# Performance work log

Measured on AMD Instinct MI355X. Metric: run time of the kernel, lower is better.

The kernel has to match this reference:

```python
import jax, jax.numpy as jnp
import numpy as np

D_STATE = 8
D_CONV = 4
DT_RANK = 8
THRESHOLD = 0.5
KPOOL = 3
PAD = (KPOOL - 1) // 2
EPS = 1e-5


def _rmsnorm(x, w):
    return x * jax.lax.rsqrt(jnp.mean(x * x, axis=-1, keepdims=True) + EPS) * w


def _dw_causal_conv(x, w, b):
    # x: (L, T, C), w: (C, 1, K) depthwise causal conv along T
    xt = jnp.transpose(x, (0, 2, 1))  # (L, C, T)
    y = jax.lax.conv_general_dilated(
        xt, w, window_strides=(1,), padding=[(D_CONV - 1, 0)],
        dimension_numbers=('NCH', 'OIH', 'NCH'), feature_group_count=xt.shape[1])
    return jnp.transpose(y, (0, 2, 1)) + b


def _selective_scan(x, delta, A, B, Cm, D):
    # x, delta: (L,T,d); A: (d,n); B, Cm: (L,T,n); D: (d,)
    dA = jnp.exp(delta[..., None] * A)                        # (L,T,d,n)
    dBx = (delta * x)[..., None] * B[:, :, None, :]           # (L,T,d,n)
    def combine(a, b):
        a1, b1 = a
        a2, b2 = b
        return (a2 * a1, a2 * b1 + b2)
    _, h = jax.lax.associative_scan(combine, (dA, dBx), axis=1)
    y = jnp.einsum('ltdn,ltn->ltd', h, Cm)
    return y + x * D


def _mamba_block(x, in_proj, conv_w, conv_b, x_proj_w, dt_proj_w, dt_proj_b,
                 A_log_f, A_log_b, D_f, D_b, out_proj_w, rms_w):
    # single-depth bidirectional (bimamba-v2 style) block, expand=1, residual + RMSNorm
    res = x
    xn = _rmsnorm(x, rms_w)
    xz = xn @ in_proj                       # (L,T,2C)
    xi, z = jnp.split(xz, 2, axis=-1)
    xi = jax.nn.silu(_dw_causal_conv(xi, conv_w, conv_b))
    dbl = xi @ x_proj_w                     # (L,T,dt_rank+2*d_state)
    dt = dbl[..., :DT_RANK]
    Bm = dbl[..., DT_RANK:DT_RANK + D_STATE]
    Cm = dbl[..., DT_RANK + D_STATE:]
    delta = jax.nn.softplus(dt @ dt_proj_w + dt_proj_b)
    A_f = -jnp.exp(A_log_f)
    A_b = -jnp.exp(A_log_b)
    flip = lambda a: a[:, ::-1]
    y_f = _selective_scan(xi, delta, A_f, Bm, Cm, D_f)
    y_b = flip(_selective_scan(flip(xi), flip(delta), A_b, flip(Bm), flip(Cm), D_b))
    y = 0.5 * (y_f + y_b) * jax.nn.silu(z)  # if_devide_out -> average two directions
    return res + y @ out_proj_w


def reference(feats, in_proj, conv_w, conv_b, x_proj_w, dt_proj_w, dt_proj_b,
              A_log_f, A_log_b, D_f, D_b, out_proj_w, rms_w, mlp_w, mlp_b,
              record_len):
    N, C, H, W = feats.shape
    T = H * W
    rec = np.asarray(record_len)  # static ragged group sizes
    ends = np.cumsum(rec)
    starts = ends - rec
    masks = []
    for s0, L in zip(starts.tolist(), rec.tolist()):
        g = feats[s0:s0 + L]                       # (L,C,H,W)
        if L > 1:
            x = g.reshape(L, C, T).transpose(0, 2, 1)  # l c h w -> l (h w) c
            feat = _mamba_block(x, in_proj, conv_w, conv_b, x_proj_w, dt_proj_w,
                                dt_proj_b, A_log_f, A_log_b, D_f, D_b,
                                out_proj_w, rms_w)
            score = jax.nn.sigmoid(feat @ mlp_w + mlp_b)   # (L,T,1)
            ego = jnp.ones((1, T, 1), feats.dtype)
            bs = jnp.concatenate([ego, score[1:]], axis=0)
        else:
            bs = jnp.ones((1, T, 1), feats.dtype)
        bs = bs.transpose(0, 2, 1).reshape(L, 1, H, W)     # l (h w) c -> l c h w
        masks.append(jnp.where(bs > THRESHOLD, 1.0, 0.0).astype(feats.dtype))
    mask = jnp.concatenate(masks, axis=0)                  # (N,1,H,W)
    pooled = jax.lax.reduce_window(
        mask, -jnp.inf, jax.lax.max,
        window_dimensions=(1, 1, KPOOL, KPOOL), window_strides=(1, 1, 1, 1),
        padding=[(0, 0), (0, 0), (PAD, PAD), (PAD, PAD)])
    return pooled


def setup_inputs():
    key = jax.random.key(0)
    ks = jax.random.split(key, 8)
    C, H, W = 128, 96, 96
    record_len = np.array([2, 3, 1, 2, 4], dtype=np.int64)
    N = int(record_len.sum())
    s = 0.05
    A_log = jnp.log(jnp.broadcast_to(
        jnp.arange(1, D_STATE + 1, dtype=jnp.float32), (C, D_STATE)))
    return {
        'feats': jax.random.normal(ks[0], (N, C, H, W), jnp.float32),
        'in_proj': jax.random.normal(ks[1], (C, 2 * C), jnp.float32) * s,
        'conv_w': jax.random.normal(ks[2], (C, 1, D_CONV), jnp.float32) * s,
        'conv_b': jnp.zeros((C,), jnp.float32),
        'x_proj_w': jax.random.normal(ks[3], (C, DT_RANK + 2 * D_STATE), jnp.float32) * s,
        'dt_proj_w': jax.random.normal(ks[4], (DT_RANK, C), jnp.float32) * s,
        'dt_proj_b': jnp.full((C,), 0.1, jnp.float32),
        'A_log_f': A_log,
        'A_log_b': A_log,
        'D_f': jnp.ones((C,), jnp.float32),
        'D_b': jnp.ones((C,), jnp.float32),
        'out_proj_w': jax.random.normal(ks[5], (C, C), jnp.float32) * s,
        'rms_w': jnp.ones((C,), jnp.float32),
        'mlp_w': jax.random.normal(ks[6], (C, 1), jnp.float32) * s,
        'mlp_b': jnp.zeros((1,), jnp.float32),
        'record_len': jnp.asarray(record_len),
    }
```

## Files before the change

kernel.cpp:

```cpp
#include <hip/hip_runtime.h>
#include <cstdint>
#include <cstddef>

#define C_CH 128
#define T_TOK 9216
#define H_IMG 96
#define W_IMG 96
#define NSTATE 8

#define CHUNK 64
#define RHALO 32
#define REGION (CHUNK + 2 * RHALO)

__device__ __forceinline__ float siluf_dev(float x) {
  return x / (1.0f + expf(-x));
}

__device__ __forceinline__ float fast_silu(float x) {
  return __fdividef(x, 1.0f + __expf(-x));
}

__global__ __launch_bounds__(128) void k0_setup(
    const int* __restrict__ rec, int n_groups, int N,
    const float* __restrict__ out_proj_w, const float* __restrict__ mlp_w,
    float* __restrict__ vvec, int* __restrict__ slot)
{
  const int tid = threadIdx.x;
  if (tid == 0) {
    int f = 0, sl = 0;
    for (int g = 0; g < n_groups; ++g) {
      const int L = rec[g];
      slot[f] = -1;
      for (int i = 1; i < L; ++i) slot[f + i] = sl++;
      f += L;
    }
  }
  if (tid < C_CH) {
    float acc = 0.0f;
    for (int j = 0; j < C_CH; ++j) acc += out_proj_w[tid * C_CH + j] * mlp_w[j];
    vvec[tid] = acc;
  }
}

__global__ __launch_bounds__(256) void k1_gemm(
    const float* __restrict__ feats, const float* __restrict__ in_proj,
    const float* __restrict__ rms_w, const float* __restrict__ mlp_w,
    const float* __restrict__ mlp_b, const float* __restrict__ vvec,
    const int* __restrict__ slot,
    float* __restrict__ xipre, float* __restrict__ wbuf,
    float* __restrict__ logit)
{
  __shared__ float Asm[C_CH * 64];
  __shared__ float Bsm[C_CH * 64];
  __shared__ float redA[256], redB[256], irS[64];
  const int f = blockIdx.y;
  const int s = slot[f];
  if (s < 0) return;
  const int m0 = blockIdx.x * 64;
  const int tid = threadIdx.x;

  {
    const int c0 = tid >> 4;
    const int tq = (tid & 15) * 4;
    const float* src = feats + (size_t)f * C_CH * T_TOK + m0 + tq;
    #pragma unroll
    for (int i = 0; i < 8; ++i) {
      const int c = c0 + i * 16;
      const float4 x4 = *(const float4*)(src + (size_t)c * T_TOK);
      *(float4*)&Asm[c * 64 + tq] = x4;
    }
  }
  __syncthreads();
  {
    const int t = tid & 63;
    const int q = tid >> 6;
    float ssum = 0.0f, rm = 0.0f;
    for (int cc = q * 32; cc < q * 32 + 32; ++cc) {
      const float val = Asm[cc * 64 + t];
      ssum += val * val;
      rm += val * mlp_w[cc];
    }
    redA[tid] = ssum; redB[tid] = rm;
  }
  __syncthreads();
  if (tid < 64) {
    const int t = tid;
    const float ssum = redA[t] + redA[t + 64] + redA[t + 128] + redA[t + 192];
    const float rm   = redB[t] + redB[t + 64] + redB[t + 128] + redB[t + 192];
    const float ir = 1.0f / sqrtf(ssum * (1.0f / C_CH) + 1e-5f);
    logit[(size_t)s * T_TOK + m0 + t] = rm + mlp_b[0];
    irS[t] = ir;
  }
  __syncthreads();
  {
    const int t = tid & 63;
    const int q = tid >> 6;
    const float ir = irS[t];
    for (int cc = q * 32; cc < q * 32 + 32; ++cc) Asm[cc * 64 + t] *= ir;
  }

  const int ti = tid >> 4;
  const int tc = tid & 15;
  for (int chunk = 0; chunk < 4; ++chunk) {
    const int n0 = chunk * 64;
    __syncthreads();
    #pragma unroll
    for (int i = 0; i < 8; ++i) {
      const int idx = tid + 256 * i;
      const int k = idx >> 4;
      const int q = (idx & 15) * 4;
      float4 b4 = *(const float4*)(in_proj + (size_t)k * 256 + n0 + q);
      const float rw = rms_w[k];
      b4.x *= rw; b4.y *= rw; b4.z *= rw; b4.w *= rw;
      *(float4*)&Bsm[k * 64 + q] = b4;
    }
    __syncthreads();
    float acc[4][4];
    #pragma unroll
    for (int i = 0; i < 4; ++i)
      #pragma unroll
      for (int j = 0; j < 4; ++j) acc[i][j] = 0.0f;
    #pragma unroll 8
    for (int k = 0; k < C_CH; ++k) {
      const float4 a4 = *(const float4*)&Asm[k * 64 + ti * 4];
      const float4 b4 = *(const float4*)&Bsm[k * 64 + tc * 4];
      acc[0][0] += a4.x * b4.x; acc[0][1] += a4.x * b4.y; acc[0][2] += a4.x * b4.z; acc[0][3] += a4.x * b4.w;
      acc[1][0] += a4.y * b4.x; acc[1][1] += a4.y * b4.y; acc[1][2] += a4.y * b4.z; acc[1][3] += a4.y * b4.w;
      acc[2][0] += a4.z * b4.x; acc[2][1] += a4.z * b4.y; acc[2][2] += a4.z * b4.z; acc[2][3] += a4.z * b4.w;
      acc[3][0] += a4.w * b4.x; acc[3][1] += a4.w * b4.y; acc[3][2] += a4.w * b4.z; acc[3][3] += a4.w * b4.w;
    }
    if (chunk < 2) {
      const int cb = n0 + tc * 4;
      #pragma unroll
      for (int i = 0; i < 4; ++i) {
        const int t = m0 + ti * 4 + i;
        float4 o; o.x = acc[i][0]; o.y = acc[i][1]; o.z = acc[i][2]; o.w = acc[i][3];
        *(float4*)&xipre[((size_t)s * T_TOK + t) * C_CH + cb] = o;
      }
    } else {
      const int zc = (chunk - 2) * 64 + tc * 4;
      const float4 v4 = *(const float4*)&vvec[zc];
      #pragma unroll
      for (int i = 0; i < 4; ++i) {
        const int t = m0 + ti * 4 + i;
        float4 o;
        o.x = 0.5f * siluf_dev(acc[i][0]) * v4.x;
        o.y = 0.5f * siluf_dev(acc[i][1]) * v4.y;
        o.z = 0.5f * siluf_dev(acc[i][2]) * v4.z;
        o.w = 0.5f * siluf_dev(acc[i][3]) * v4.w;
        *(float4*)&wbuf[((size_t)s * T_TOK + t) * C_CH + zc] = o;
      }
    }
  }
}

__global__ __launch_bounds__(256, 4) void k2_convproj(
    const float* __restrict__ xipre,
    const float* __restrict__ conv_w, const float* __restrict__ conv_b,
    const float* __restrict__ x_proj_w, const int* __restrict__ slot,
    float* __restrict__ dbl_g)
{
  __shared__ float xibuf[64 * 129];
  const int f = blockIdx.y;
  const int s = slot[f];
  if (s < 0) return;
  const int m0 = blockIdx.x * 64;
  const int tid = threadIdx.x;
  const int c = tid & 127;
  const int half = tid >> 7;
  const size_t rowbase = (size_t)s * T_TOK;
  const float4 cw = *(const float4*)(conv_w + c * 4);
  const float cb = conv_b[c];

  auto ldx = [&](int t) -> float {
    return (t >= 0) ? xipre[(rowbase + t) * C_CH + c] : 0.0f;
  };

  {
    const int t0 = m0 + half * 32;
    float xm1 = ldx(t0 - 1), xm2 = ldx(t0 - 2), xm3 = ldx(t0 - 3);
    #pragma unroll
    for (int i = 0; i < 32; ++i) {
      const float cur = ldx(t0 + i);
      const float sum = cw.x * xm3 + cw.y * xm2 + cw.z * xm1 + cw.w * cur + cb;
      xibuf[(half * 32 + i) * 129 + c] = fast_silu(sum);
      xm3 = xm2; xm2 = xm1; xm1 = cur;
    }
  }
  __syncthreads();
  {
    const int q6 = __builtin_amdgcn_readfirstlane(tid >> 6) * 6;
    const int tok = tid & 63;
    float acc[6] = {0, 0, 0, 0, 0, 0};
    for (int cc = 0; cc < C_CH; ++cc) {
      const float xv = xibuf[tok * 129 + cc];
      #pragma unroll
      for (int jj = 0; jj < 6; ++jj)
        acc[jj] += xv * x_proj_w[cc * 24 + q6 + jj];
    }
    #pragma unroll
    for (int jj = 0; jj < 6; ++jj)
      dbl_g[(rowbase + m0 + tok) * 24 + q6 + jj] = acc[jj];
  }
}

__global__ __launch_bounds__(256, 4) void k3_scan(
    const float* __restrict__ xipre, const float* __restrict__ wbuf,
    const float* __restrict__ dbl_g,
    const float* __restrict__ conv_w, const float* __restrict__ conv_b,
    const float* __restrict__ dt_proj_w, const float* __restrict__ dt_proj_b,
    const float* __restrict__ A_log_f, const float* __restrict__ A_log_b,
    const float* __restrict__ D_f, const float* __restrict__ D_b,
    const int* __restrict__ slot, float* __restrict__ logit)
{
  __shared__ float dbl[REGION * 24];
  const int f = blockIdx.y;
  const int s = slot[f];
  if (s < 0) return;
  const int c0 = blockIdx.x * CHUNK;
  const int r0 = c0 - RHALO;
  const int tid = threadIdx.x;
  const int c = tid & 127;
  const int half = tid >> 7;
  const size_t rowbase = (size_t)s * T_TOK;
  const float4 cw = *(const float4*)(conv_w + c * 4);
  const float cb = conv_b[c];

  auto ldx = [&](int t) -> float {
    return (t >= 0 && t < T_TOK) ? xipre[(rowbase + t) * C_CH + c] : 0.0f;
  };

  {
    const long grow = ((long)rowbase + r0) * 24;
    const int lo  = (r0 < 0) ? (-r0) * 6 : 0;
    const int hi  = (r0 + REGION > T_TOK) ? (T_TOK - r0) * 6 : REGION * 6;
    #pragma unroll
    for (int i = 0; i < 3; ++i) {
      const int idx = tid + i * 256;
      if (idx >= lo && idx < hi)
        *(float4*)&dbl[idx * 4] = *(const float4*)&dbl_g[grow + (long)idx * 4];
    }
  }
  __syncthreads();

  float dw[8], Ac[8];
  const float* Alog = half ? A_log_b : A_log_f;
  #pragma unroll
  for (int r = 0; r < 8; ++r) dw[r] = dt_proj_w[r * C_CH + c];
  #pragma unroll
  for (int n = 0; n < NSTATE; ++n) Ac[n] = -expf(Alog[c * NSTATE + n]);
  const float bias = dt_proj_b[c];
  const float Dd = half ? D_b[c] : D_f[c];
  float h[8] = {0, 0, 0, 0, 0, 0, 0, 0};

  const float a0 = Ac[0];
  int okl = 1;
  #pragma unroll
  for (int n = 1; n < NSTATE; ++n)
    okl &= (fabsf(Ac[n] - (float)(n + 1) * a0) <= 1e-4f * fabsf(Ac[n])) ? 1 : 0;
  const bool fastA = (__all(okl) != 0);

  auto decay8 = [&](float dlt, float* dA) {
    if (fastA) {
      const float e1 = __expf(dlt * a0);
      const float e2 = e1 * e1, e3 = e2 * e1, e4 = e2 * e2;
      dA[0] = e1; dA[1] = e2; dA[2] = e3; dA[3] = e4;
      dA[4] = e4 * e1; dA[5] = e4 * e2; dA[6] = e4 * e3; dA[7] = e4 * e4;
    } else {
      #pragma unroll
      for (int n = 0; n < NSTATE; ++n) dA[n] = __expf(dlt * Ac[n]);
    }
  };

  if (half == 0) {
    const int tb = (r0 < 0) ? 0 : r0;
    const int steps = c0 + CHUNK - tb;
    const int outg0 = (c0 - tb) >> 3;
    const int ng = steps >> 3;
    float xm1 = ldx(tb - 1), xm2 = ldx(tb - 2), xm3 = ldx(tb - 3);
    for (int g = 0; g < ng; ++g) {
      const int t0 = tb + g * 8;
      const bool out = (g >= outg0);
      float pg[8], wg[8];
      #pragma unroll
      for (int j = 0; j < 8; ++j) {
        const size_t gi = (rowbase + t0 + j) * C_CH + c;
        pg[j] = xipre[gi];
        wg[j] = out ? wbuf[gi] : 0.0f;
      }
      #pragma unroll
      for (int j = 0; j < 8; ++j) {
        const int t = t0 + j;
        const int p = t - r0;
        const float cur = pg[j];
        const float sum = cw.x * xm3 + cw.y * xm2 + cw.z * xm1 + cw.w * cur + cb;
        const float xiv = fast_silu(sum);
        xm3 = xm2; xm2 = xm1; xm1 = cur;
        const float4 d0 = *(const float4*)&dbl[p * 24];
        const float4 d1 = *(const float4*)&dbl[p * 24 + 4];
        float pre = bias;
        pre += d0.x * dw[0] + d0.y * dw[1] + d0.z * dw[2] + d0.w * dw[3];
        pre += d1.x * dw[4] + d1.y * dw[5] + d1.z * dw[6] + d1.w * dw[7];
        const float dlt = fmaxf(pre, 0.0f) + __logf(1.0f + __expf(-fabsf(pre)));
        const float u = dlt * xiv;
        const float4 b0 = *(const float4*)&dbl[p * 24 + 8];
        const float4 b1 = *(const float4*)&dbl[p * 24 + 12];
        float dA[8];
        decay8(dlt, dA);
        h[0] = dA[0] * h[0] + u * b0.x;
        h[1] = dA[1] * h[1] + u * b0.y;
        h[2] = dA[2] * h[2] + u * b0.z;
        h[3] = dA[3] * h[3] + u * b0.w;
        h[4] = dA[4] * h[4] + u * b1.x;
        h[5] = dA[5] * h[5] + u * b1.y;
        h[6] = dA[6] * h[6] + u * b1.z;
        h[7] = dA[7] * h[7] + u * b1.w;
        if (out) {
          const float4 cc0 = *(const float4*)&dbl[p * 24 + 16];
          const float4 cc1 = *(const float4*)&dbl[p * 24 + 20];
          float y = xiv * Dd;
          y += h[0] * cc0.x + h[1] * cc0.y + h[2] * cc0.z + h[3] * cc0.w;
          y += h[4] * cc1.x + h[5] * cc1.y + h[6] * cc1.z + h[7] * cc1.w;
          float contrib = y * wg[j];
          contrib += __shfl_xor(contrib, 1);
          contrib += __shfl_xor(contrib, 2);
          contrib += __shfl_xor(contrib, 4);
          contrib += __shfl_xor(contrib, 8);
          contrib += __shfl_xor(contrib, 16);
          contrib += __shfl_xor(contrib, 32);
          if ((tid & 63) == 0) atomicAdd(&logit[rowbase + t], contrib);
        }
      }
    }
  } else {
    const int te2e = r0 + REGION;
    const int te2 = (te2e > T_TOK) ? T_TOK : te2e;
    const int steps = te2 - c0;
    const int outg0 = (te2 - (c0 + CHUNK)) >> 3;
    const int ng = steps >> 3;
    float w0 = ldx(te2 - 1), w1 = ldx(te2 - 2), w2 = ldx(te2 - 3), w3 = ldx(te2 - 4);
    for (int g = 0; g < ng; ++g) {
      const int t0 = te2 - 1 - g * 8;
      const bool out = (g >= outg0);
      float nv[8], wg[8];
      #pragma unroll
      for (int j = 0; j < 8; ++j) {
        nv[j] = ldx(t0 - 4 - j);
        wg[j] = out ? wbuf[(rowbase + t0 - j) * C_CH + c] : 0.0f;
      }
      #pragma unroll
      for (int j = 0; j < 8; ++j) {
        const int t = t0 - j;
        const int p = t - r0;
        const float sum = cw.x * w3 + cw.y * w2 + cw.z * w1 + cw.w * w0 + cb;
        const float xiv = fast_silu(sum);
        w0 = w1; w1 = w2; w2 = w3; w3 = nv[j];
        const float4 d0 = *(const float4*)&dbl[p * 24];
        const float4 d1 = *(const float4*)&dbl[p * 24 + 4];
        float pre = bias;
        pre += d0.x * dw[0] + d0.y * dw[1] + d0.z * dw[2] + d0.w * dw[3];
        pre += d1.x * dw[4] + d1.y * dw[5] + d1.z * dw[6] + d1.w * dw[7];
        const float dlt = fmaxf(pre, 0.0f) + __logf(1.0f + __expf(-fabsf(pre)));
        const float u = dlt * xiv;
        const float4 b0 = *(const float4*)&dbl[p * 24 + 8];
        const float4 b1 = *(const float4*)&dbl[p * 24 + 12];
        float dA[8];
        decay8(dlt, dA);
        h[0] = dA[0] * h[0] + u * b0.x;
        h[1] = dA[1] * h[1] + u * b0.y;
        h[2] = dA[2] * h[2] + u * b0.z;
        h[3] = dA[3] * h[3] + u * b0.w;
        h[4] = dA[4] * h[4] + u * b1.x;
        h[5] = dA[5] * h[5] + u * b1.y;
        h[6] = dA[6] * h[6] + u * b1.z;
        h[7] = dA[7] * h[7] + u * b1.w;
        if (out) {
          const float4 cc0 = *(const float4*)&dbl[p * 24 + 16];
          const float4 cc1 = *(const float4*)&dbl[p * 24 + 20];
          float y = xiv * Dd;
          y += h[0] * cc0.x + h[1] * cc0.y + h[2] * cc0.z + h[3] * cc0.w;
          y += h[4] * cc1.x + h[5] * cc1.y + h[6] * cc1.z + h[7] * cc1.w;
          float contrib = y * wg[j];
          contrib += __shfl_xor(contrib, 1);
          contrib += __shfl_xor(contrib, 2);
          contrib += __shfl_xor(contrib, 4);
          contrib += __shfl_xor(contrib, 8);
          contrib += __shfl_xor(contrib, 16);
          contrib += __shfl_xor(contrib, 32);
          if ((tid & 63) == 0) atomicAdd(&logit[rowbase + t], contrib);
        }
      }
    }
  }
}

__global__ __launch_bounds__(128) void k4_pool(
    const float* __restrict__ logit, const int* __restrict__ slot,
    float* __restrict__ out)
{
  const int w = threadIdx.x;
  if (w >= W_IMG) return;
  const int hh = blockIdx.x;
  const int f = blockIdx.y;
  const int s = slot[f];
  float m = 0.0f;
  if (s < 0) {
    m = 1.0f;
  } else {
    for (int dh = -1; dh <= 1; ++dh) {
      const int h2 = hh + dh;
      if (h2 < 0 || h2 >= H_IMG) continue;
      for (int dw = -1; dw <= 1; ++dw) {
        const int w2 = w + dw;
        if (w2 < 0 || w2 >= W_IMG) continue;
        if (logit[(size_t)s * T_TOK + h2 * W_IMG + w2] > 0.0f) m = 1.0f;
      }
    }
  }
  out[(size_t)f * T_TOK + hh * W_IMG + w] = m;
}

extern "C" void kernel_launch(void* const* d_in, const int* in_sizes, int n_in,
                              void* d_out, int out_size, void* d_ws, size_t ws_size,
                              hipStream_t stream) {
  const float* feats      = (const float*)d_in[0];
  const float* in_proj    = (const float*)d_in[1];
  const float* conv_w     = (const float*)d_in[2];
  const float* conv_b     = (const float*)d_in[3];
  const float* x_proj_w   = (const float*)d_in[4];
  const float* dt_proj_w  = (const float*)d_in[5];
  const float* dt_proj_b  = (const float*)d_in[6];
  const float* A_log_f    = (const float*)d_in[7];
  const float* A_log_b    = (const float*)d_in[8];
  const float* D_f        = (const float*)d_in[9];
  const float* D_b        = (const float*)d_in[10];
  const float* out_proj_w = (const float*)d_in[11];
  const float* rms_w      = (const float*)d_in[12];
  const float* mlp_w      = (const float*)d_in[13];
  const float* mlp_b      = (const float*)d_in[14];
  const int*   rec        = (const int*)d_in[15];

  const int N = in_sizes[0] / (C_CH * T_TOK);
  const int n_groups = in_sizes[15];
  int S = N - n_groups;
  if (S < 1) S = 1;

  char* p = (char*)d_ws;
  float* vvec  = (float*)p; p += 1024;
  int*   slot  = (int*)p;   p += ((N * 4 + 255) / 256) * 256;
  float* logit = (float*)p; p += (size_t)S * T_TOK * 4;
  float* xipre = (float*)p; p += (size_t)S * T_TOK * C_CH * 4;
  float* wA    = (float*)p; p += (size_t)S * T_TOK * C_CH * 4;
  float* dblg  = (float*)p; p += (size_t)S * T_TOK * 24 * 4;
  (void)ws_size; (void)n_in; (void)out_size;

  k0_setup<<<1, 128, 0, stream>>>(rec, n_groups, N, out_proj_w, mlp_w, vvec, slot);
  k1_gemm<<<dim3(T_TOK / 64, N), 256, 0, stream>>>(
      feats, in_proj, rms_w, mlp_w, mlp_b, vvec, slot, xipre, wA, logit);
  k2_convproj<<<dim3(T_TOK / 64, N), 256, 0, stream>>>(
      xipre, conv_w, conv_b, x_proj_w, slot, dblg);
  k3_scan<<<dim3(T_TOK / CHUNK, N), 256, 0, stream>>>(
      xipre, wA, dblg, conv_w, conv_b, dt_proj_w, dt_proj_b,
      A_log_f, A_log_b, D_f, D_b, slot, logit);
  k4_pool<<<dim3(H_IMG, N), 128, 0, stream>>>(logit, slot, (float*)d_out);
}
```

Baseline: 323.3 us.

## Split scan directions across blocks, double-buffer scan loads, drop GEMM B staging

The scan kernel now runs forward and backward directions as separate 128-thread blocks along a grid z dimension instead of two halves of one 256-thread block. Its per-group global loads are double-buffered so the next 8-token group is fetched while the current one is processed. The input-projection GEMM stops staging in_proj in shared memory; it folds rms_w into the A tile and reads B directly from global/L2, freeing shared memory for higher occupancy. The risks are higher register pressure from the doubled load buffers and more global traffic per FMA in the GEMM.

```diff
diff --git a/kernel.cpp b/kernel.cpp
--- a/kernel.cpp
+++ b/kernel.cpp
@@ -42,7 +42,7 @@
   }
 }
 
-__global__ __launch_bounds__(256) void k1_gemm(
+__global__ __launch_bounds__(256, 4) void k1_gemm(
     const float* __restrict__ feats, const float* __restrict__ in_proj,
     const float* __restrict__ rms_w, const float* __restrict__ mlp_w,
     const float* __restrict__ mlp_b, const float* __restrict__ vvec,
@@ -51,7 +51,6 @@
     float* __restrict__ logit)
 {
   __shared__ float Asm[C_CH * 64];
-  __shared__ float Bsm[C_CH * 64];
   __shared__ float redA[256], redB[256], irS[64];
   const int f = blockIdx.y;
   const int s = slot[f];
@@ -96,25 +95,16 @@
     const int t = tid & 63;
     const int q = tid >> 6;
     const float ir = irS[t];
-    for (int cc = q * 32; cc < q * 32 + 32; ++cc) Asm[cc * 64 + t] *= ir;
-  }
+    for (int cc = q * 32; cc < q * 32 + 32; ++cc)
+      Asm[cc * 64 + t] = (Asm[cc * 64 + t] * ir) * rms_w[cc];
+  }
+  __syncthreads();
 
   const int ti = tid >> 4;
   const int tc = tid & 15;
   for (int chunk = 0; chunk < 4; ++chunk) {
     const int n0 = chunk * 64;
-    __syncthreads();
-    #pragma unroll
-    for (int i = 0; i < 8; ++i) {
-      const int idx = tid + 256 * i;
-      const int k = idx >> 4;
-      const int q = (idx & 15) * 4;
-      float4 b4 = *(const float4*)(in_proj + (size_t)k * 256 + n0 + q);
-      const float rw = rms_w[k];
-      b4.x *= rw; b4.y *= rw; b4.z *= rw; b4.w *= rw;
-      *(float4*)&Bsm[k * 64 + q] = b4;
-    }
-    __syncthreads();
+    const float* bp = in_proj + n0 + tc * 4;
     float acc[4][4];
     #pragma unroll
     for (int i = 0; i < 4; ++i)
@@ -123,7 +113,7 @@
     #pragma unroll 8
     for (int k = 0; k < C_CH; ++k) {
       const float4 a4 = *(const float4*)&Asm[k * 64 + ti * 4];
-      const float4 b4 = *(const float4*)&Bsm[k * 64 + tc * 4];
+      const float4 b4 = *(const float4*)(bp + (size_t)k * 256);
       acc[0][0] += a4.x * b4.x; acc[0][1] += a4.x * b4.y; acc[0][2] += a4.x * b4.z; acc[0][3] += a4.x * b4.w;
       acc[1][0] += a4.y * b4.x; acc[1][1] += a4.y * b4.y; acc[1][2] += a4.y * b4.z; acc[1][3] += a4.y * b4.w;
       acc[2][0] += a4.z * b4.x; acc[2][1] += a4.z * b4.y; acc[2][2] += a4.z * b4.z; acc[2][3] += a4.z * b4.w;
@@ -204,7 +194,7 @@
   }
 }
 
-__global__ __launch_bounds__(256, 4) void k3_scan(
+__global__ __launch_bounds__(128, 4) void k3_scan(
     const float* __restrict__ xipre, const float* __restrict__ wbuf,
     const float* __restrict__ dbl_g,
     const float* __restrict__ conv_w, const float* __restrict__ conv_b,
@@ -220,8 +210,8 @@
   const int c0 = blockIdx.x * CHUNK;
   const int r0 = c0 - RHALO;
   const int tid = threadIdx.x;
-  const int c = tid & 127;
-  const int half = tid >> 7;
+  const int c = tid;
+  const int half = blockIdx.z;
   const size_t rowbase = (size_t)s * T_TOK;
   const float4 cw = *(const float4*)(conv_w + c * 4);
   const float cb = conv_b[c];
@@ -235,8 +225,8 @@
     const int lo  = (r0 < 0) ? (-r0) * 6 : 0;
     const int hi  = (r0 + REGION > T_TOK) ? (T_TOK - r0) * 6 : REGION * 6;
     #pragma unroll
-    for (int i = 0; i < 3; ++i) {
-      const int idx = tid + i * 256;
+    for (int i = 0; i < 6; ++i) {
+      const int idx = tid + i * 128;
       if (idx >= lo && idx < hi)
         *(float4*)&dbl[idx * 4] = *(const float4*)&dbl_g[grow + (long)idx * 4];
     }
@@ -272,126 +262,123 @@
     }
   };
 
+#define SCAN_CORE(P_, XIV_, OUT_, WGJ_, T_) do {                              \
+    const float4 d0 = *(const float4*)&dbl[(P_) * 24];                        \
+    const float4 d1 = *(const float4*)&dbl[(P_) * 24 + 4];                    \
+    float pre = bias;                                                         \
+    pre += d0.x * dw[0] + d0.y * dw[1] + d0.z * dw[2] + d0.w * dw[3];         \
+    pre += d1.x * dw[4] + d1.y * dw[5] + d1.z * dw[6] + d1.w * dw[7];         \
+    const float dlt = fmaxf(pre, 0.0f) + __logf(1.0f + __expf(-fabsf(pre)));  \
+    const float u = dlt * (XIV_);                                             \
+    const float4 b0 = *(const float4*)&dbl[(P_) * 24 + 8];                    \
+    const float4 b1 = *(const float4*)&dbl[(P_) * 24 + 12];                   \
+    float dA[8];                                                              \
+    decay8(dlt, dA);                                                          \
+    h[0] = dA[0] * h[0] + u * b0.x;                                           \
+    h[1] = dA[1] * h[1] + u * b0.y;                                           \
+    h[2] = dA[2] * h[2] + u * b0.z;                                           \
+    h[3] = dA[3] * h[3] + u * b0.w;                                           \
+    h[4] = dA[4] * h[4] + u * b1.x;                                           \
+    h[5] = dA[5] * h[5] + u * b1.y;                                           \
+    h[6] = dA[6] * h[6] + u * b1.z;                                           \
+    h[7] = dA[7] * h[7] + u * b1.w;                                           \
+    if (OUT_) {                                                               \
+      const float4 cc0 = *(const float4*)&dbl[(P_) * 24 + 16];                \
+      const float4 cc1 = *(const float4*)&dbl[(P_) * 24 + 20];                \
+      float y = (XIV_) * Dd;                                                  \
+      y += h[0] * cc0.x + h[1] * cc0.y + h[2] * cc0.z + h[3] * cc0.w;         \
+      y += h[4] * cc1.x + h[5] * cc1.y + h[6] * cc1.z + h[7] * cc1.w;         \
+      float contrib = y * (WGJ_);                                             \
+      contrib += __shfl_xor(contrib, 1);                                      \
+      contrib += __shfl_xor(contrib, 2);                                      \
+      contrib += __shfl_xor(contrib, 4);                                      \
+      contrib += __shfl_xor(contrib, 8);                                      \
+      contrib += __shfl_xor(contrib, 16);                                     \
+      contrib += __shfl_xor(contrib, 32);                                     \
+      if ((tid & 63) == 0) atomicAdd(&logit[rowbase + (T_)], contrib);        \
+    } } while (0)
+
   if (half == 0) {
     const int tb = (r0 < 0) ? 0 : r0;
-    const int steps = c0 + CHUNK - tb;
     const int outg0 = (c0 - tb) >> 3;
-    const int ng = steps >> 3;
+    const int ng = (c0 + CHUNK - tb) >> 3;
     float xm1 = ldx(tb - 1), xm2 = ldx(tb - 2), xm3 = ldx(tb - 3);
-    for (int g = 0; g < ng; ++g) {
-      const int t0 = tb + g * 8;
-      const bool out = (g >= outg0);
-      float pg[8], wg[8];
-      #pragma unroll
-      for (int j = 0; j < 8; ++j) {
-        const size_t gi = (rowbase + t0 + j) * C_CH + c;
-        pg[j] = xipre[gi];
-        wg[j] = out ? wbuf[gi] : 0.0f;
-      }
-      #pragma unroll
-      for (int j = 0; j < 8; ++j) {
-        const int t = t0 + j;
-        const int p = t - r0;
-        const float cur = pg[j];
-        const float sum = cw.x * xm3 + cw.y * xm2 + cw.z * xm1 + cw.w * cur + cb;
-        const float xiv = fast_silu(sum);
-        xm3 = xm2; xm2 = xm1; xm1 = cur;
-        const float4 d0 = *(const float4*)&dbl[p * 24];
-        const float4 d1 = *(const float4*)&dbl[p * 24 + 4];
-        float pre = bias;
-        pre += d0.x * dw[0] + d0.y * dw[1] + d0.z * dw[2] + d0.w * dw[3];
-        pre += d1.x * dw[4] + d1.y * dw[5] + d1.z * dw[6] + d1.w * dw[7];
-        const float dlt = fmaxf(pre, 0.0f) + __logf(1.0f + __expf(-fabsf(pre)));
-        const float u = dlt * xiv;
-        const float4 b0 = *(const float4*)&dbl[p * 24 + 8];
-        const float4 b1 = *(const float4*)&dbl[p * 24 + 12];
-        float dA[8];
-        decay8(dlt, dA);
-        h[0] = dA[0] * h[0] + u * b0.x;
-        h[1] = dA[1] * h[1] + u * b0.y;
-        h[2] = dA[2] * h[2] + u * b0.z;
-        h[3] = dA[3] * h[3] + u * b0.w;
-        h[4] = dA[4] * h[4] + u * b1.x;
-        h[5] = dA[5] * h[5] + u * b1.y;
-        h[6] = dA[6] * h[6] + u * b1.z;
-        h[7] = dA[7] * h[7] + u * b1.w;
-        if (out) {
-          const float4 cc0 = *(const float4*)&dbl[p * 24 + 16];
-          const float4 cc1 = *(const float4*)&dbl[p * 24 + 20];
-          float y = xiv * Dd;
-          y += h[0] * cc0.x + h[1] * cc0.y + h[2] * cc0.z + h[3] * cc0.w;
-          y += h[4] * cc1.x + h[5] * cc1.y + h[6] * cc1.z + h[7] * cc1.w;
-          float contrib = y * wg[j];
-          contrib += __shfl_xor(contrib, 1);
-          contrib += __shfl_xor(contrib, 2);
-          contrib += __shfl_xor(contrib, 4);
-          contrib += __shfl_xor(contrib, 8);
-          contrib += __shfl_xor(contrib, 16);
-          contrib += __shfl_xor(contrib, 32);
-          if ((tid & 63) == 0) atomicAdd(&logit[rowbase + t], contrib);
-        }
-      }
+    float pgA[8], wgA[8], pgB[8], wgB[8];
+
+#define LOADF(G, PG, WG) do {                                                 \
+    const int t0_ = tb + (G) * 8;                                             \
+    const bool out_ = ((G) >= outg0);                                         \
+    _Pragma("unroll")                                                         \
+    for (int j = 0; j < 8; ++j) {                                             \
+      const size_t gi = (rowbase + t0_ + j) * C_CH + c;                       \
+      PG[j] = xipre[gi];                                                      \
+      WG[j] = out_ ? wbuf[gi] : 0.0f;                                         \
+    } } while (0)
+
+#define STEPSF(G, PG, WG) do {                                                \
+    const int t0_ = tb + (G) * 8;                                             \
+    const bool out_ = ((G) >= outg0);                                         \
+    _Pragma("unroll")                                                         \
+    for (int j = 0; j < 8; ++j) {                                             \
+      const int t = t0_ + j;                                                  \
+      const int p = t - r0;                                                   \
+      const float cur = PG[j];                                                \
+      const float sum = cw.x * xm3 + cw.y * xm2 + cw.z * xm1 + cw.w * cur + cb; \
+      const float xiv = fast_silu(sum);                                       \
+      xm3 = xm2; xm2 = xm1; xm1 = cur;                                        \
+      SCAN_CORE(p, xiv, out_, WG[j], t);                                      \
+    } } while (0)
+
+    LOADF(0, pgA, wgA);
+    for (int g = 0; g < ng; g += 2) {
+      LOADF(g + 1, pgB, wgB);
+      STEPSF(g, pgA, wgA);
+      if (g + 2 < ng) LOADF(g + 2, pgA, wgA);
+      STEPSF(g + 1, pgB, wgB);
     }
   } else {
     const int te2e = r0 + REGION;
     const int te2 = (te2e > T_TOK) ? T_TOK : te2e;
-    const int steps = te2 - c0;
     const int outg0 = (te2 - (c0 + CHUNK)) >> 3;
-    const int ng = steps >> 3;
+    const int ng = (te2 - c0) >> 3;
     float w0 = ldx(te2 - 1), w1 = ldx(te2 - 2), w2 = ldx(te2 - 3), w3 = ldx(te2 - 4);
-    for (int g = 0; g < ng; ++g) {
-      const int t0 = te2 - 1 - g * 8;
-      const bool out = (g >= outg0);
-      float nv[8], wg[8];
-      #pragma unroll
-      for (int j = 0; j < 8; ++j) {
-        nv[j] = ldx(t0 - 4 - j);
-        wg[j] = out ? wbuf[(rowbase + t0 - j) * C_CH + c] : 0.0f;
-      }
-      #pragma unroll
-      for (int j = 0; j < 8; ++j) {
-        const int t = t0 - j;
-        const int p = t - r0;
-        const float sum = cw.x * w3 + cw.y * w2 + cw.z * w1 + cw.w * w0 + cb;
-        const float xiv = fast_silu(sum);
-        w0 = w1; w1 = w2; w2 = w3; w3 = nv[j];
-        const float4 d0 = *(const float4*)&dbl[p * 24];
-        const float4 d1 = *(const float4*)&dbl[p * 24 + 4];
-        float pre = bias;
-        pre += d0.x * dw[0] + d0.y * dw[1] + d0.z * dw[2] + d0.w * dw[3];
-        pre += d1.x * dw[4] + d1.y * dw[5] + d1.z * dw[6] + d1.w * dw[7];
-        const float dlt = fmaxf(pre, 0.0f) + __logf(1.0f + __expf(-fabsf(pre)));
-        const float u = dlt * xiv;
-        const float4 b0 = *(const float4*)&dbl[p * 24 + 8];
-        const float4 b1 = *(const float4*)&dbl[p * 24 + 12];
-        float dA[8];
-        decay8(dlt, dA);
-        h[0] = dA[0] * h[0] + u * b0.x;
-        h[1] = dA[1] * h[1] + u * b0.y;
-        h[2] = dA[2] * h[2] + u * b0.z;
-        h[3] = dA[3] * h[3] + u * b0.w;
-        h[4] = dA[4] * h[4] + u * b1.x;
-        h[5] = dA[5] * h[5] + u * b1.y;
-        h[6] = dA[6] * h[6] + u * b1.z;
-        h[7] = dA[7] * h[7] + u * b1.w;
-        if (out) {
-          const float4 cc0 = *(const float4*)&dbl[p * 24 + 16];
-          const float4 cc1 = *(const float4*)&dbl[p * 24 + 20];
-          float y = xiv * Dd;
-          y += h[0] * cc0.x + h[1] * cc0.y + h[2] * cc0.z + h[3] * cc0.w;
-          y += h[4] * cc1.x + h[5] * cc1.y + h[6] * cc1.z + h[7] * cc1.w;
-          float contrib = y * wg[j];
-          contrib += __shfl_xor(contrib, 1);
-          contrib += __shfl_xor(contrib, 2);
-          contrib += __shfl_xor(contrib, 4);
-          contrib += __shfl_xor(contrib, 8);
-          contrib += __shfl_xor(contrib, 16);
-          contrib += __shfl_xor(contrib, 32);
-          if ((tid & 63) == 0) atomicAdd(&logit[rowbase + t], contrib);
-        }
-      }
-    }
-  }
+    float pgA[8], wgA[8], pgB[8], wgB[8];
+
+#define LOADB(G, NV, WG) do {                                                 \
+    const int t0_ = te2 - 1 - (G) * 8;                                        \
+    const bool out_ = ((G) >= outg0);                                         \
+    _Pragma("unroll")                                                         \
+    for (int j = 0; j < 8; ++j) {                                             \
+      NV[j] = ldx(t0_ - 4 - j);                                               \
+      WG[j] = out_ ? wbuf[(rowbase + t0_ - j) * C_CH + c] : 0.0f;             \
+    } } while (0)
+
+#define STEPSB(G, NV, WG) do {                                                \
+    const int t0_ = te2 - 1 - (G) * 8;                                        \
+    const bool out_ = ((G) >= outg0);                                         \
+    _Pragma("unroll")                                                         \
+    for (int j = 0; j < 8; ++j) {                                             \
+      const int t = t0_ - j;                                                  \
+      const int p = t - r0;                                                   \
+      const float sum = cw.x * w3 + cw.y * w2 + cw.z * w1 + cw.w * w0 + cb;   \
+      const float xiv = fast_silu(sum);                                       \
+      w0 = w1; w1 = w2; w2 = w3; w3 = NV[j];                                  \
+      SCAN_CORE(p, xiv, out_, WG[j], t);                                      \
+    } } while (0)
+
+    LOADB(0, pgA, wgA);
+    for (int g = 0; g < ng; g += 2) {
+      LOADB(g + 1, pgB, wgB);
+      STEPSB(g, pgA, wgA);
+      if (g + 2 < ng) LOADB(g + 2, pgA, wgA);
+      STEPSB(g + 1, pgB, wgB);
+    }
+  }
+#undef SCAN_CORE
+#undef LOADF
+#undef STEPSF
+#undef LOADB
+#undef STEPSB
 }
 
 __global__ __launch_bounds__(128) void k4_pool(
@@ -459,7 +446,7 @@
       feats, in_proj, rms_w, mlp_w, mlp_b, vvec, slot, xipre, wA, logit);
   k2_convproj<<<dim3(T_TOK / 64, N), 256, 0, stream>>>(
       xipre, conv_w, conv_b, x_proj_w, slot, dblg);
-  k3_scan<<<dim3(T_TOK / CHUNK, N), 256, 0, stream>>>(
+  k3_scan<<<dim3(T_TOK / CHUNK, N, 2), 128, 0, stream>>>(
       xipre, wA, dblg, conv_w, conv_b, dt_proj_w, dt_proj_b,
       A_log_f, A_log_b, D_f, D_b, slot, logit);
   k4_pool<<<dim3(H_IMG, N), 128, 0, stream>>>(logit, slot, (float*)d_out);
```

Result: slower. 351.6 us (+8.7%).
